# Kernel optimization log

Measured on AMD Instinct MI355X. Metric: run time of the kernel, lower is better.

## Reference

```python
import jax, jax.numpy as jnp
import numpy as np

ALPHA = 1.0
BETA = 1.0
NUM_BIAS_CLASSES = 2


def setup_inputs() -> dict:
    key = jax.random.key(0)
    k1, k2, k3, k4 = jax.random.split(key, 4)
    N, C, D = 4096, 10, 2048
    logits = jax.random.normal(k1, (N, C), dtype=jnp.float32)
    labels = jax.random.randint(k2, (N,), 0, C)
    biases = jax.random.randint(k3, (N,), 0, NUM_BIAS_CLASSES)
    feats = jax.random.normal(k4, (N, D), dtype=jnp.float32)
    return {"logits": logits, "labels": labels, "biases": biases, "feats": feats}


def reference(logits, labels, biases, feats):
    N = feats.shape[0]
    f32 = jnp.float32

    # ----- cross entropy (mean reduction, matches F.cross_entropy) -----
    logp = jax.nn.log_softmax(logits, axis=-1)
    label_loss = -jnp.mean(jnp.take_along_axis(logp, labels[:, None], axis=1))

    # ----- gram matrix: strict lower triangle of feats @ feats.T, clamped -----
    idx = jnp.arange(N)
    strict_lower = idx[:, None] > idx[None, :]            # [N, N] bool, i > j
    gram = jnp.matmul(feats, feats.T)                     # [N, N]
    gram = jnp.clip(jnp.where(strict_lower, gram, 0.0), -1.0, 1.0)

    # ----- R_ortho: per-bias-class |sum of gram over same-bias strict-lower pairs| -----
    # S_b = sum_{i>j, bias_i=bias_j=b} gram_ij = m_b^T gram m_b  (gram already strict lower)
    B = jax.nn.one_hot(biases, NUM_BIAS_CLASSES, dtype=f32)  # [N, NB]
    S = jnp.einsum('ib,ij,jb->b', B, gram, B)                # [NB]
    counts = jnp.sum(B, axis=0)                              # n_b per bias class
    M = counts * (counts - 1.0) * 0.5                        # strict-lower same-bias pairs
    M_tot_o = jnp.sum(M)
    # if M_b == 0 then S_b == 0, so summing all |S_b| matches the torch loop
    R_ortho = jnp.where(M_tot_o > 0, jnp.sum(jnp.abs(S)) / M_tot_o, 0.0)

    # ----- R_parallel: pairs i>j, same target, bias_i < bias_j (unique() is sorted,
    # so row-bias is the earlier-indexed class and col-bias the later one) -----
    same_target = labels[:, None] == labels[None, :]
    bias_lt = biases[:, None] < biases[None, :]
    pmask = (strict_lower & same_target & bias_lt).astype(f32)
    M_tot_p = jnp.sum(pmask)
    ploss = -0.5 * jnp.sum((1.0 + gram) * pmask)
    R_parallel = jnp.where(M_tot_p > 0, 1.0 + ploss / M_tot_p, 0.0)

    bias_loss = ALPHA * R_ortho + BETA * R_parallel
    return (label_loss, bias_loss)
```

## Files before the change

### kernel.cpp

```cpp
#include <hip/hip_runtime.h>
#include <hip/hip_bf16.h>

typedef short  bf16x8 __attribute__((ext_vector_type(8)));
typedef float  f32x4  __attribute__((ext_vector_type(4)));
typedef unsigned int uint2v __attribute__((ext_vector_type(2)));
typedef unsigned short ushort_t;

#define GLD_LDS16(gp, lp) __builtin_amdgcn_global_load_lds(                 \
    (const __attribute__((address_space(1))) void*)(gp),                    \
    (__attribute__((address_space(3))) void*)(lp), 16, 0, 0)

static __device__ inline short f2bf(float x) {
    unsigned u = __builtin_bit_cast(unsigned, x);
    u += 0x7fffu + ((u >> 16) & 1u);
    return (short)(u >> 16);
}

__global__ __launch_bounds__(256)
void convert_swz8_kernel(const float* __restrict__ in,
                         unsigned char* __restrict__ out,
                         int N, int D)
{
    int uid = blockIdx.x * blockDim.x + threadIdx.x;
    int nw  = D >> 3;
    if (uid >= N * nw) return;
    int row = uid / nw;
    int w   = uid - row * nw;
    int kt  = w >> 3;
    int p   = w & 7;
    int f   = p ^ (row & 7);
    int k   = kt * 64 + ((f >> 2) << 5) + ((f & 3) << 3);
    const float* s = in + (size_t)row * D + k;
    f32x4 a = *(const f32x4*)s;
    f32x4 b = *(const f32x4*)(s + 4);
    unsigned lo = __builtin_amdgcn_cvt_pk_fp8_f32(a[0], a[1], 0, 0);
    lo = __builtin_amdgcn_cvt_pk_fp8_f32(a[2], a[3], lo, 1);
    unsigned hi = __builtin_amdgcn_cvt_pk_fp8_f32(b[0], b[1], 0, 0);
    hi = __builtin_amdgcn_cvt_pk_fp8_f32(b[2], b[3], hi, 1);
    uint2v v = {lo, hi};
    *(uint2v*)(out + (size_t)uid * 8) = v;
}

__global__ __launch_bounds__(512, 1)
void gram_8phase8_kernel(const unsigned char* __restrict__ fb,
                         const int* __restrict__ labels,
                         const int* __restrict__ biases,
                         float* __restrict__ accbuf,
                         int N, int D)
{
    __shared__ unsigned char As[3][2][128][64];
    __shared__ unsigned char Bs[3][2][128][64];
    __shared__ int lab_r[256], bia_r[256], lab_c[256], bia_c[256];

    int nt = N >> 8;
    int b  = blockIdx.x;
    int nwg = gridDim.x;
    if ((nwg & 7) == 0) b = (b & 7) * (nwg >> 3) + (b >> 3);
    int r = b / nt, c = b % nt;
    int rowbase = r * 256, colbase = c * 256;

    int tid = threadIdx.x;
    if (tid < 256) {
        lab_r[tid] = labels[rowbase + tid];
        bia_r[tid] = biases[rowbase + tid];
    } else {
        int u = tid - 256;
        lab_c[u] = labels[colbase + u];
        bia_c[u] = biases[colbase + u];
    }

    int lane = tid & 63;
    int wid  = tid >> 6;
    int wr   = wid >> 2;
    int wc   = wid & 3;
    int lrow = lane & 15;
    int kgrp = lane >> 4;

    auto STAGE_A = [&](int slot, int h, int kt) {
        int row = tid >> 2;
        int blk = tid & 3;
        const unsigned char* g =
            fb + (size_t)(rowbase + h * 128 + row) * D + kt * 64 + blk * 16;
        GLD_LDS16(g, &As[slot][h][0][0] + tid * 16);
    };
    auto STAGE_B = [&](int slot, int h, int kt) {
        int row = tid >> 2;
        int blk = tid & 3;
        const unsigned char* g =
            fb + (size_t)(colbase + h * 128 + row) * D + kt * 64 + blk * 16;
        GLD_LDS16(g, &Bs[slot][h][0][0] + tid * 16);
    };

    f32x4 acc[8][4] = {};
    int nkt = D >> 6;

    STAGE_A(0, 0, 0); STAGE_A(0, 1, 0); STAGE_B(0, 0, 0); STAGE_B(0, 1, 0);
    STAGE_A(1, 0, 1); STAGE_A(1, 1, 1); STAGE_B(1, 0, 1); STAGE_B(1, 1, 1);
    asm volatile("s_waitcnt vmcnt(4)" ::: "memory");
    __builtin_amdgcn_s_barrier();

    int hb  = wc >> 1;
    int lcb = (wc & 1) * 64;

    int slot = 0, s2 = 2;
    for (int kt = 0; kt < nkt; ++kt) {
        int stg = (kt + 2 < nkt);
        unsigned long breg[4][2];

        #pragma unroll
        for (int q = 0; q < 4; ++q) {
            if (q == 0) {
                #pragma unroll
                for (int n = 0; n < 4; ++n)
                    #pragma unroll
                    for (int ks = 0; ks < 2; ++ks) {
                        int lc = lcb + n * 16 + lrow;
                        int u  = (ks * 4 + kgrp) ^ (lc & 7);
                        breg[n][ks] = *(const unsigned long*)(
                            &Bs[slot][hb][lc][0] + u * 8);
                    }
            }
            unsigned long areg[2][2];
            #pragma unroll
            for (int mm = 0; mm < 2; ++mm)
                #pragma unroll
                for (int ks = 0; ks < 2; ++ks) {
                    int lr = (q * 2 + mm) * 16 + lrow;
                    int u  = (ks * 4 + kgrp) ^ (lr & 7);
                    areg[mm][ks] = *(const unsigned long*)(
                        &As[slot][wr][lr][0] + u * 8);
                }
            if (stg) {
                if (q == 0)      STAGE_A(s2, 0, kt + 2);
                else if (q == 1) STAGE_A(s2, 1, kt + 2);
                else if (q == 2) STAGE_B(s2, 0, kt + 2);
                else             STAGE_B(s2, 1, kt + 2);
            }
            if (q == 3) {
                if (stg)
                    asm volatile("s_waitcnt vmcnt(4)" ::: "memory");
                else
                    asm volatile("s_waitcnt vmcnt(0)" ::: "memory");
            }
            __builtin_amdgcn_s_barrier();
            asm volatile("s_waitcnt lgkmcnt(0)" ::: "memory");
            __builtin_amdgcn_s_setprio(1);
            #pragma unroll
            for (int mm = 0; mm < 2; ++mm)
                #pragma unroll
                for (int n = 0; n < 4; ++n)
                    #pragma unroll
                    for (int ks = 0; ks < 2; ++ks)
                        acc[q * 2 + mm][n] =
                            __builtin_amdgcn_mfma_f32_16x16x32_fp8_fp8(
                                (long)areg[mm][ks], (long)breg[n][ks],
                                acc[q * 2 + mm][n], 0, 0, 0);
            __builtin_amdgcn_s_setprio(0);
            __builtin_amdgcn_s_barrier();
        }

        slot = (slot == 2) ? 0 : slot + 1;
        s2   = (s2   == 2) ? 0 : s2 + 1;
    }

    if (r < c) return;

    float s0 = 0.f, s1 = 0.f, ps = 0.f, pc = 0.f;
    #pragma unroll
    for (int m = 0; m < 8; ++m) {
        #pragma unroll
        for (int e = 0; e < 4; ++e) {
            int li = wr * 128 + m * 16 + kgrp * 4 + e;
            int gi = rowbase + li;
            int labi = lab_r[li];
            int bi   = bia_r[li];
            #pragma unroll
            for (int n = 0; n < 4; ++n) {
                int lj = wc * 64 + n * 16 + lrow;
                int gj = colbase + lj;
                if (gi > gj) {
                    float g = acc[m][n][e];
                    g = fminf(fmaxf(g, -1.f), 1.f);
                    int bj = bia_c[lj];
                    if (bi == bj) {
                        if (bi == 0) s0 += g; else s1 += g;
                    } else if (labi == lab_c[lj] && bi < bj) {
                        ps += 1.f + g;
                        pc += 1.f;
                    }
                }
            }
        }
    }
    #pragma unroll
    for (int off = 32; off > 0; off >>= 1) {
        s0 += __shfl_down(s0, off);
        s1 += __shfl_down(s1, off);
        ps += __shfl_down(ps, off);
        pc += __shfl_down(pc, off);
    }
    if (lane == 0) {
        atomicAdd(&accbuf[0], s0);
        atomicAdd(&accbuf[1], s1);
        atomicAdd(&accbuf[2], ps);
        atomicAdd(&accbuf[3], pc);
    }
}

__global__ __launch_bounds__(256, 2)
void gram_fused_kernel(const float* __restrict__ feats,
                       const int* __restrict__ labels,
                       const int* __restrict__ biases,
                       float* __restrict__ accbuf,
                       int N, int D)
{
    __shared__ ushort_t As[128 * 64];
    __shared__ ushort_t Bs[128 * 64];
    __shared__ int lab_r[128], bia_r[128], lab_c[128], bia_c[128];

    int t = blockIdx.x;
    int r = (int)((sqrtf(8.0f * (float)t + 1.0f) - 1.0f) * 0.5f);
    while ((r + 1) * (r + 2) / 2 <= t) ++r;
    while (r * (r + 1) / 2 > t) --r;
    int c = t - r * (r + 1) / 2;
    int rowbase = r * 128, colbase = c * 128;

    int tid = threadIdx.x;
    if (tid < 128) {
        lab_r[tid] = labels[rowbase + tid];
        bia_r[tid] = biases[rowbase + tid];
    } else {
        int u = tid - 128;
        lab_c[u] = labels[colbase + u];
        bia_c[u] = biases[colbase + u];
    }

    int lane = tid & 63;
    int wid  = tid >> 6;
    int wr   = wid >> 1;
    int wc   = wid & 1;
    int lrow = lane & 15;
    int kgrp = lane >> 4;

    f32x4 acc[4][4] = {};

    for (int k0 = 0; k0 < D; k0 += 64) {
        __syncthreads();
        #pragma unroll
        for (int it = 0; it < 4; ++it) {
            int wlin = tid + it * 256;
            int row  = wlin >> 3;
            int kc   = wlin & 7;
            const float* ga = feats + (size_t)(rowbase + row) * D + k0 + kc * 8;
            const float* gb = feats + (size_t)(colbase + row) * D + k0 + kc * 8;
            f32x4 a0 = *(const f32x4*)ga;
            f32x4 a1 = *(const f32x4*)(ga + 4);
            f32x4 b0 = *(const f32x4*)gb;
            f32x4 b1 = *(const f32x4*)(gb + 4);
            bf16x8 av, bv;
            #pragma unroll
            for (int e = 0; e < 4; ++e) {
                av[e]     = f2bf(a0[e]);
                av[e + 4] = f2bf(a1[e]);
                bv[e]     = f2bf(b0[e]);
                bv[e + 4] = f2bf(b1[e]);
            }
            int boff = row * 128 + ((kc * 16) ^ ((row & 7) << 4));
            *(bf16x8*)((char*)As + boff) = av;
            *(bf16x8*)((char*)Bs + boff) = bv;
        }
        __syncthreads();

        #pragma unroll
        for (int kk = 0; kk < 2; ++kk) {
            bf16x8 a[4], bb[4];
            #pragma unroll
            for (int m = 0; m < 4; ++m) {
                int rr = wr * 64 + m * 16 + lrow;
                int off = rr * 128 + ((kk * 64 + kgrp * 16) ^ ((rr & 7) << 4));
                a[m] = *(const bf16x8*)((const char*)As + off);
            }
            #pragma unroll
            for (int n = 0; n < 4; ++n) {
                int cc = wc * 64 + n * 16 + lrow;
                int off = cc * 128 + ((kk * 64 + kgrp * 16) ^ ((cc & 7) << 4));
                bb[n] = *(const bf16x8*)((const char*)Bs + off);
            }
            #pragma unroll
            for (int m = 0; m < 4; ++m)
                #pragma unroll
                for (int n = 0; n < 4; ++n)
                    acc[m][n] = __builtin_amdgcn_mfma_f32_16x16x32_bf16(
                        a[m], bb[n], acc[m][n], 0, 0, 0);
        }
    }

    float s0 = 0.f, s1 = 0.f, ps = 0.f, pc = 0.f;
    #pragma unroll
    for (int m = 0; m < 4; ++m) {
        #pragma unroll
        for (int e = 0; e < 4; ++e) {
            int li = wr * 64 + m * 16 + kgrp * 4 + e;
            int gi = rowbase + li;
            int labi = lab_r[li];
            int bi   = bia_r[li];
            #pragma unroll
            for (int n = 0; n < 4; ++n) {
                int lj = wc * 64 + n * 16 + lrow;
                int gj = colbase + lj;
                if (gi > gj) {
                    float g = acc[m][n][e];
                    g = fminf(fmaxf(g, -1.f), 1.f);
                    int bj = bia_c[lj];
                    if (bi == bj) {
                        if (bi == 0) s0 += g; else s1 += g;
                    } else if (labi == lab_c[lj] && bi < bj) {
                        ps += 1.f + g;
                        pc += 1.f;
                    }
                }
            }
        }
    }
    #pragma unroll
    for (int off = 32; off > 0; off >>= 1) {
        s0 += __shfl_down(s0, off);
        s1 += __shfl_down(s1, off);
        ps += __shfl_down(ps, off);
        pc += __shfl_down(pc, off);
    }
    if (lane == 0) {
        atomicAdd(&accbuf[0], s0);
        atomicAdd(&accbuf[1], s1);
        atomicAdd(&accbuf[2], ps);
        atomicAdd(&accbuf[3], pc);
    }
}

__global__ __launch_bounds__(256)
void ce_count_kernel(const float* __restrict__ logits,
                     const int* __restrict__ labels,
                     const int* __restrict__ biases,
                     float* __restrict__ accbuf,
                     int N, int C)
{
    int i = blockIdx.x * blockDim.x + threadIdx.x;
    float loss = 0.f, c0 = 0.f, c1 = 0.f;
    if (i < N) {
        const float* row = logits + (size_t)i * C;
        float mx = -INFINITY;
        for (int k = 0; k < C; ++k) mx = fmaxf(mx, row[k]);
        float s = 0.f;
        for (int k = 0; k < C; ++k) s += expf(row[k] - mx);
        loss = mx + logf(s) - row[labels[i]];
        if (biases[i] == 0) c0 = 1.f; else c1 = 1.f;
    }
    #pragma unroll
    for (int off = 32; off > 0; off >>= 1) {
        loss += __shfl_down(loss, off);
        c0   += __shfl_down(c0, off);
        c1   += __shfl_down(c1, off);
    }
    if ((threadIdx.x & 63) == 0) {
        atomicAdd(&accbuf[4], loss);
        atomicAdd(&accbuf[5], c0);
        atomicAdd(&accbuf[6], c1);
    }
}

__global__ void finalize_kernel(const float* __restrict__ accbuf,
                                float* __restrict__ out, int N)
{
    float S0 = accbuf[0], S1 = accbuf[1], ps = accbuf[2], pc = accbuf[3];
    float ce = accbuf[4], n0 = accbuf[5], n1 = accbuf[6];
    float Mo = 0.5f * (n0 * (n0 - 1.f) + n1 * (n1 - 1.f));
    float Ro = (Mo > 0.f) ? (fabsf(S0) + fabsf(S1)) / Mo : 0.f;
    float Rp = (pc > 0.f) ? 1.f + (-0.5f * ps) / pc : 0.f;
    out[0] = ce / (float)N;
    out[1] = Ro + Rp;
}

extern "C" void kernel_launch(void* const* d_in, const int* in_sizes, int n_in,
                              void* d_out, int out_size, void* d_ws, size_t ws_size,
                              hipStream_t stream)
{
    const float* logits = (const float*)d_in[0];
    const int*   labels = (const int*)d_in[1];
    const int*   biases = (const int*)d_in[2];
    const float* feats  = (const float*)d_in[3];

    int N = in_sizes[1];
    int C = in_sizes[0] / N;
    int D = in_sizes[3] / N;

    float* accbuf = (float*)d_ws;
    hipMemsetAsync(accbuf, 0, 8 * sizeof(float), stream);

    size_t need = 256 + (size_t)N * D;
    if (ws_size >= need && (N & 255) == 0 && (D & 127) == 0) {
        unsigned char* fb = (unsigned char*)d_ws + 256;
        int nu = N * (D >> 3);
        convert_swz8_kernel<<<(nu + 255) / 256, 256, 0, stream>>>(feats, fb,
                                                                  N, D);
        int nt = N >> 8;
        gram_8phase8_kernel<<<nt * nt, 512, 0, stream>>>(fb, labels, biases,
                                                         accbuf, N, D);
    } else {
        int nt = N / 128;
        int T  = nt * (nt + 1) / 2;
        gram_fused_kernel<<<T, 256, 0, stream>>>(feats, labels, biases, accbuf,
                                                 N, D);
    }
    ce_count_kernel<<<(N + 255) / 256, 256, 0, stream>>>(logits, labels, biases,
                                                         accbuf, N, C);
    finalize_kernel<<<1, 1, 0, stream>>>(accbuf, (float*)d_out, N);
}
```

Baseline: 142.6 us.

## Retile gram kernel to 256x128 blocks with 128-wide K steps

```diff
diff --git a/kernel.cpp b/kernel.cpp
--- a/kernel.cpp
+++ b/kernel.cpp
@@ -26,10 +26,10 @@
     if (uid >= N * nw) return;
     int row = uid / nw;
     int w   = uid - row * nw;
-    int kt  = w >> 3;
-    int p   = w & 7;
-    int f   = p ^ (row & 7);
-    int k   = kt * 64 + ((f >> 2) << 5) + ((f & 3) << 3);
+    int P   = w >> 4;
+    int p   = w & 15;
+    int f   = p ^ (row & 15);
+    int k   = P * 128 + ((f >> 2) << 5) + ((f & 3) << 3);
     const float* s = in + (size_t)row * D + k;
     f32x4 a = *(const f32x4*)s;
     f32x4 b = *(const f32x4*)(s + 4);
@@ -42,28 +42,28 @@
 }
 
 __global__ __launch_bounds__(512, 1)
-void gram_8phase8_kernel(const unsigned char* __restrict__ fb,
-                         const int* __restrict__ labels,
-                         const int* __restrict__ biases,
-                         float* __restrict__ accbuf,
-                         int N, int D)
-{
-    __shared__ unsigned char As[3][2][128][64];
-    __shared__ unsigned char Bs[3][2][128][64];
-    __shared__ int lab_r[256], bia_r[256], lab_c[256], bia_c[256];
-
-    int nt = N >> 8;
+void gram_p2_kernel(const unsigned char* __restrict__ fb,
+                    const int* __restrict__ labels,
+                    const int* __restrict__ biases,
+                    float* __restrict__ accbuf,
+                    int N, int D)
+{
+    __shared__ unsigned char As[3][256 * 128];
+    __shared__ unsigned char Bs[3][128 * 128];
+    __shared__ int lab_r[256], bia_r[256], lab_c[128], bia_c[128];
+
+    int nc = N >> 7;
     int b  = blockIdx.x;
     int nwg = gridDim.x;
     if ((nwg & 7) == 0) b = (b & 7) * (nwg >> 3) + (b >> 3);
-    int r = b / nt, c = b % nt;
-    int rowbase = r * 256, colbase = c * 256;
+    int r = b / nc, c = b % nc;
+    int rowbase = r * 256, colbase = c * 128;
 
     int tid = threadIdx.x;
     if (tid < 256) {
         lab_r[tid] = labels[rowbase + tid];
         bia_r[tid] = biases[rowbase + tid];
-    } else {
+    } else if (tid < 384) {
         int u = tid - 256;
         lab_c[u] = labels[colbase + u];
         bia_c[u] = biases[colbase + u];
@@ -71,106 +71,121 @@
 
     int lane = tid & 63;
     int wid  = tid >> 6;
-    int wr   = wid >> 2;
-    int wc   = wid & 3;
+    int wr   = wid >> 1;
+    int wc   = wid & 1;
     int lrow = lane & 15;
     int kgrp = lane >> 4;
 
-    auto STAGE_A = [&](int slot, int h, int kt) {
-        int row = tid >> 2;
-        int blk = tid & 3;
+    auto STAGE_A = [&](int slot, int kt, int i) {
+        int j   = i * 512 + tid;
+        int row = j >> 3;
+        int blk = j & 7;
         const unsigned char* g =
-            fb + (size_t)(rowbase + h * 128 + row) * D + kt * 64 + blk * 16;
-        GLD_LDS16(g, &As[slot][h][0][0] + tid * 16);
+            fb + (size_t)(rowbase + row) * D + kt * 128 + blk * 16;
+        GLD_LDS16(g, &As[slot][0] + j * 16);
     };
-    auto STAGE_B = [&](int slot, int h, int kt) {
-        int row = tid >> 2;
-        int blk = tid & 3;
+    auto STAGE_B = [&](int slot, int kt, int i) {
+        int j   = i * 512 + tid;
+        int row = j >> 3;
+        int blk = j & 7;
         const unsigned char* g =
-            fb + (size_t)(colbase + h * 128 + row) * D + kt * 64 + blk * 16;
-        GLD_LDS16(g, &Bs[slot][h][0][0] + tid * 16);
+            fb + (size_t)(colbase + row) * D + kt * 128 + blk * 16;
+        GLD_LDS16(g, &Bs[slot][0] + j * 16);
     };
 
-    f32x4 acc[8][4] = {};
-    int nkt = D >> 6;
-
-    STAGE_A(0, 0, 0); STAGE_A(0, 1, 0); STAGE_B(0, 0, 0); STAGE_B(0, 1, 0);
-    STAGE_A(1, 0, 1); STAGE_A(1, 1, 1); STAGE_B(1, 0, 1); STAGE_B(1, 1, 1);
-    asm volatile("s_waitcnt vmcnt(4)" ::: "memory");
+    f32x4 acc[4][4] = {};
+    int nkt = D >> 7;
+
+    STAGE_A(0, 0, 0); STAGE_A(0, 0, 1); STAGE_A(0, 0, 2); STAGE_A(0, 0, 3);
+    STAGE_B(0, 0, 0); STAGE_B(0, 0, 1);
+    STAGE_A(1, 1, 0); STAGE_A(1, 1, 1); STAGE_A(1, 1, 2); STAGE_A(1, 1, 3);
+    STAGE_B(1, 1, 0); STAGE_B(1, 1, 1);
+    asm volatile("s_waitcnt vmcnt(6)" ::: "memory");
     __builtin_amdgcn_s_barrier();
-
-    int hb  = wc >> 1;
-    int lcb = (wc & 1) * 64;
 
     int slot = 0, s2 = 2;
     for (int kt = 0; kt < nkt; ++kt) {
         int stg = (kt + 2 < nkt);
-        unsigned long breg[4][2];
-
-        #pragma unroll
-        for (int q = 0; q < 4; ++q) {
-            if (q == 0) {
+        unsigned long breg[4][4];
+        const unsigned char* Ab = &As[slot][0];
+        const unsigned char* Bb = &Bs[slot][0];
+
+        #pragma unroll
+        for (int n = 0; n < 4; ++n)
+            #pragma unroll
+            for (int ks = 0; ks < 4; ++ks) {
+                int lc = wc * 64 + n * 16 + lrow;
+                int u  = (ks * 4 + kgrp) ^ (lc & 15);
+                breg[n][ks] = *(const unsigned long*)(Bb + lc * 128 + u * 8);
+            }
+        unsigned long a0[2][4];
+        #pragma unroll
+        for (int mm = 0; mm < 2; ++mm)
+            #pragma unroll
+            for (int ks = 0; ks < 4; ++ks) {
+                int lr = wr * 64 + mm * 16 + lrow;
+                int u  = (ks * 4 + kgrp) ^ (lr & 15);
+                a0[mm][ks] = *(const unsigned long*)(Ab + lr * 128 + u * 8);
+            }
+        if (stg) { STAGE_A(s2, kt + 2, 0); STAGE_A(s2, kt + 2, 1);
+                   STAGE_A(s2, kt + 2, 2); }
+        __builtin_amdgcn_s_barrier();
+        asm volatile("s_waitcnt lgkmcnt(0)" ::: "memory");
+        __builtin_amdgcn_s_setprio(1);
+        #pragma unroll
+        for (int mm = 0; mm < 2; ++mm)
+            #pragma unroll
+            for (int n = 0; n < 4; ++n)
                 #pragma unroll
-                for (int n = 0; n < 4; ++n)
-                    #pragma unroll
-                    for (int ks = 0; ks < 2; ++ks) {
-                        int lc = lcb + n * 16 + lrow;
-                        int u  = (ks * 4 + kgrp) ^ (lc & 7);
-                        breg[n][ks] = *(const unsigned long*)(
-                            &Bs[slot][hb][lc][0] + u * 8);
-                    }
-            }
-            unsigned long areg[2][2];
-            #pragma unroll
-            for (int mm = 0; mm < 2; ++mm)
+                for (int ks = 0; ks < 4; ++ks)
+                    acc[mm][n] = __builtin_amdgcn_mfma_f32_16x16x32_fp8_fp8(
+                        (long)a0[mm][ks], (long)breg[n][ks], acc[mm][n],
+                        0, 0, 0);
+        __builtin_amdgcn_s_setprio(0);
+        __builtin_amdgcn_s_barrier();
+
+        unsigned long a1[2][4];
+        #pragma unroll
+        for (int mm = 0; mm < 2; ++mm)
+            #pragma unroll
+            for (int ks = 0; ks < 4; ++ks) {
+                int lr = wr * 64 + (2 + mm) * 16 + lrow;
+                int u  = (ks * 4 + kgrp) ^ (lr & 15);
+                a1[mm][ks] = *(const unsigned long*)(Ab + lr * 128 + u * 8);
+            }
+        if (stg) { STAGE_A(s2, kt + 2, 3); STAGE_B(s2, kt + 2, 0);
+                   STAGE_B(s2, kt + 2, 1); }
+        if (stg)
+            asm volatile("s_waitcnt vmcnt(6)" ::: "memory");
+        else
+            asm volatile("s_waitcnt vmcnt(0)" ::: "memory");
+        __builtin_amdgcn_s_barrier();
+        asm volatile("s_waitcnt lgkmcnt(0)" ::: "memory");
+        __builtin_amdgcn_s_setprio(1);
+        #pragma unroll
+        for (int mm = 0; mm < 2; ++mm)
+            #pragma unroll
+            for (int n = 0; n < 4; ++n)
                 #pragma unroll
-                for (int ks = 0; ks < 2; ++ks) {
-                    int lr = (q * 2 + mm) * 16 + lrow;
-                    int u  = (ks * 4 + kgrp) ^ (lr & 7);
-                    areg[mm][ks] = *(const unsigned long*)(
-                        &As[slot][wr][lr][0] + u * 8);
-                }
-            if (stg) {
-                if (q == 0)      STAGE_A(s2, 0, kt + 2);
-                else if (q == 1) STAGE_A(s2, 1, kt + 2);
-                else if (q == 2) STAGE_B(s2, 0, kt + 2);
-                else             STAGE_B(s2, 1, kt + 2);
-            }
-            if (q == 3) {
-                if (stg)
-                    asm volatile("s_waitcnt vmcnt(4)" ::: "memory");
-                else
-                    asm volatile("s_waitcnt vmcnt(0)" ::: "memory");
-            }
-            __builtin_amdgcn_s_barrier();
-            asm volatile("s_waitcnt lgkmcnt(0)" ::: "memory");
-            __builtin_amdgcn_s_setprio(1);
-            #pragma unroll
-            for (int mm = 0; mm < 2; ++mm)
-                #pragma unroll
-                for (int n = 0; n < 4; ++n)
-                    #pragma unroll
-                    for (int ks = 0; ks < 2; ++ks)
-                        acc[q * 2 + mm][n] =
-                            __builtin_amdgcn_mfma_f32_16x16x32_fp8_fp8(
-                                (long)areg[mm][ks], (long)breg[n][ks],
-                                acc[q * 2 + mm][n], 0, 0, 0);
-            __builtin_amdgcn_s_setprio(0);
-            __builtin_amdgcn_s_barrier();
-        }
+                for (int ks = 0; ks < 4; ++ks)
+                    acc[2 + mm][n] = __builtin_amdgcn_mfma_f32_16x16x32_fp8_fp8(
+                        (long)a1[mm][ks], (long)breg[n][ks], acc[2 + mm][n],
+                        0, 0, 0);
+        __builtin_amdgcn_s_setprio(0);
+        __builtin_amdgcn_s_barrier();
 
         slot = (slot == 2) ? 0 : slot + 1;
         s2   = (s2   == 2) ? 0 : s2 + 1;
     }
 
-    if (r < c) return;
+    if (rowbase + 255 <= colbase) return;
 
     float s0 = 0.f, s1 = 0.f, ps = 0.f, pc = 0.f;
     #pragma unroll
-    for (int m = 0; m < 8; ++m) {
+    for (int m = 0; m < 4; ++m) {
         #pragma unroll
         for (int e = 0; e < 4; ++e) {
-            int li = wr * 128 + m * 16 + kgrp * 4 + e;
+            int li = wr * 64 + m * 16 + kgrp * 4 + e;
             int gi = rowbase + li;
             int labi = lab_r[li];
             int bi   = bia_r[li];
@@ -402,9 +417,10 @@
         int nu = N * (D >> 3);
         convert_swz8_kernel<<<(nu + 255) / 256, 256, 0, stream>>>(feats, fb,
                                                                   N, D);
-        int nt = N >> 8;
-        gram_8phase8_kernel<<<nt * nt, 512, 0, stream>>>(fb, labels, biases,
-                                                         accbuf, N, D);
+        int nr = N >> 8;
+        int nc = N >> 7;
+        gram_p2_kernel<<<nr * nc, 512, 0, stream>>>(fb, labels, biases,
+                                                    accbuf, N, D);
     } else {
         int nt = N / 128;
         int T  = nt * (nt + 1) / 2;
```

Measured after the change: 178.9 us. 1.25x slower.

## Pair fp8 k-groups into 16-byte LDS reads and use a two-phase k-loop

Applied to the files above, without the earlier changes.

```diff
diff --git a/kernel.cpp b/kernel.cpp
--- a/kernel.cpp
+++ b/kernel.cpp
@@ -3,7 +3,8 @@
 
 typedef short  bf16x8 __attribute__((ext_vector_type(8)));
 typedef float  f32x4  __attribute__((ext_vector_type(4)));
-typedef unsigned int uint2v __attribute__((ext_vector_type(2)));
+typedef unsigned int uint4v __attribute__((ext_vector_type(4)));
+typedef unsigned long u64x2 __attribute__((ext_vector_type(2)));
 typedef unsigned short ushort_t;
 
 #define GLD_LDS16(gp, lp) __builtin_amdgcn_global_load_lds(                 \
@@ -17,36 +18,41 @@
 }
 
 __global__ __launch_bounds__(256)
-void convert_swz8_kernel(const float* __restrict__ in,
-                         unsigned char* __restrict__ out,
-                         int N, int D)
+void convert_pair8_kernel(const float* __restrict__ in,
+                          unsigned char* __restrict__ out,
+                          int N, int D)
 {
     int uid = blockIdx.x * blockDim.x + threadIdx.x;
-    int nw  = D >> 3;
+    int nw  = D >> 4;
     if (uid >= N * nw) return;
     int row = uid / nw;
     int w   = uid - row * nw;
-    int kt  = w >> 3;
-    int p   = w & 7;
-    int f   = p ^ (row & 7);
-    int k   = kt * 64 + ((f >> 2) << 5) + ((f & 3) << 3);
-    const float* s = in + (size_t)row * D + k;
-    f32x4 a = *(const f32x4*)s;
-    f32x4 b = *(const f32x4*)(s + 4);
-    unsigned lo = __builtin_amdgcn_cvt_pk_fp8_f32(a[0], a[1], 0, 0);
-    lo = __builtin_amdgcn_cvt_pk_fp8_f32(a[2], a[3], lo, 1);
-    unsigned hi = __builtin_amdgcn_cvt_pk_fp8_f32(b[0], b[1], 0, 0);
-    hi = __builtin_amdgcn_cvt_pk_fp8_f32(b[2], b[3], hi, 1);
-    uint2v v = {lo, hi};
-    *(uint2v*)(out + (size_t)uid * 8) = v;
+    int kt  = w >> 2;
+    int g   = w & 3;
+    int k0  = kt * 64 + g * 8;
+    const float* s = in + (size_t)row * D + k0;
+    f32x4 a0 = *(const f32x4*)s;
+    f32x4 a1 = *(const f32x4*)(s + 4);
+    f32x4 b0 = *(const f32x4*)(s + 32);
+    f32x4 b1 = *(const f32x4*)(s + 36);
+    unsigned w0 = __builtin_amdgcn_cvt_pk_fp8_f32(a0[0], a0[1], 0, 0);
+    w0 = __builtin_amdgcn_cvt_pk_fp8_f32(a0[2], a0[3], w0, 1);
+    unsigned w1 = __builtin_amdgcn_cvt_pk_fp8_f32(a1[0], a1[1], 0, 0);
+    w1 = __builtin_amdgcn_cvt_pk_fp8_f32(a1[2], a1[3], w1, 1);
+    unsigned w2 = __builtin_amdgcn_cvt_pk_fp8_f32(b0[0], b0[1], 0, 0);
+    w2 = __builtin_amdgcn_cvt_pk_fp8_f32(b0[2], b0[3], w2, 1);
+    unsigned w3 = __builtin_amdgcn_cvt_pk_fp8_f32(b1[0], b1[1], 0, 0);
+    w3 = __builtin_amdgcn_cvt_pk_fp8_f32(b1[2], b1[3], w3, 1);
+    uint4v v = {w0, w1, w2, w3};
+    *(uint4v*)(out + (size_t)uid * 16) = v;
 }
 
 __global__ __launch_bounds__(512, 1)
-void gram_8phase8_kernel(const unsigned char* __restrict__ fb,
-                         const int* __restrict__ labels,
-                         const int* __restrict__ biases,
-                         float* __restrict__ accbuf,
-                         int N, int D)
+void gram_p2k64_kernel(const unsigned char* __restrict__ fb,
+                       const int* __restrict__ labels,
+                       const int* __restrict__ biases,
+                       float* __restrict__ accbuf,
+                       int N, int D)
 {
     __shared__ unsigned char As[3][2][128][64];
     __shared__ unsigned char Bs[3][2][128][64];
@@ -105,59 +111,60 @@
     int slot = 0, s2 = 2;
     for (int kt = 0; kt < nkt; ++kt) {
         int stg = (kt + 2 < nkt);
-        unsigned long breg[4][2];
-
-        #pragma unroll
-        for (int q = 0; q < 4; ++q) {
-            if (q == 0) {
-                #pragma unroll
-                for (int n = 0; n < 4; ++n)
-                    #pragma unroll
-                    for (int ks = 0; ks < 2; ++ks) {
-                        int lc = lcb + n * 16 + lrow;
-                        int u  = (ks * 4 + kgrp) ^ (lc & 7);
-                        breg[n][ks] = *(const unsigned long*)(
-                            &Bs[slot][hb][lc][0] + u * 8);
-                    }
-            }
-            unsigned long areg[2][2];
-            #pragma unroll
-            for (int mm = 0; mm < 2; ++mm)
-                #pragma unroll
-                for (int ks = 0; ks < 2; ++ks) {
-                    int lr = (q * 2 + mm) * 16 + lrow;
-                    int u  = (ks * 4 + kgrp) ^ (lr & 7);
-                    areg[mm][ks] = *(const unsigned long*)(
-                        &As[slot][wr][lr][0] + u * 8);
-                }
-            if (stg) {
-                if (q == 0)      STAGE_A(s2, 0, kt + 2);
-                else if (q == 1) STAGE_A(s2, 1, kt + 2);
-                else if (q == 2) STAGE_B(s2, 0, kt + 2);
-                else             STAGE_B(s2, 1, kt + 2);
-            }
-            if (q == 3) {
-                if (stg)
-                    asm volatile("s_waitcnt vmcnt(4)" ::: "memory");
-                else
-                    asm volatile("s_waitcnt vmcnt(0)" ::: "memory");
-            }
-            __builtin_amdgcn_s_barrier();
-            asm volatile("s_waitcnt lgkmcnt(0)" ::: "memory");
-            __builtin_amdgcn_s_setprio(1);
-            #pragma unroll
-            for (int mm = 0; mm < 2; ++mm)
-                #pragma unroll
-                for (int n = 0; n < 4; ++n)
-                    #pragma unroll
-                    for (int ks = 0; ks < 2; ++ks)
-                        acc[q * 2 + mm][n] =
-                            __builtin_amdgcn_mfma_f32_16x16x32_fp8_fp8(
-                                (long)areg[mm][ks], (long)breg[n][ks],
-                                acc[q * 2 + mm][n], 0, 0, 0);
-            __builtin_amdgcn_s_setprio(0);
-            __builtin_amdgcn_s_barrier();
-        }
+        u64x2 breg[4];
+
+        #pragma unroll
+        for (int n = 0; n < 4; ++n) {
+            int lc = lcb + n * 16 + lrow;
+            breg[n] = *(const u64x2*)(&Bs[slot][hb][lc][0] + kgrp * 16);
+        }
+        u64x2 a0[4];
+        #pragma unroll
+        for (int mm = 0; mm < 4; ++mm) {
+            int lr = mm * 16 + lrow;
+            a0[mm] = *(const u64x2*)(&As[slot][wr][lr][0] + kgrp * 16);
+        }
+        if (stg) { STAGE_A(s2, 0, kt + 2); STAGE_A(s2, 1, kt + 2); }
+        __builtin_amdgcn_s_barrier();
+        asm volatile("s_waitcnt lgkmcnt(0)" ::: "memory");
+        __builtin_amdgcn_s_setprio(1);
+        #pragma unroll
+        for (int mm = 0; mm < 4; ++mm)
+            #pragma unroll
+            for (int n = 0; n < 4; ++n) {
+                acc[mm][n] = __builtin_amdgcn_mfma_f32_16x16x32_fp8_fp8(
+                    (long)a0[mm][0], (long)breg[n][0], acc[mm][n], 0, 0, 0);
+                acc[mm][n] = __builtin_amdgcn_mfma_f32_16x16x32_fp8_fp8(
+                    (long)a0[mm][1], (long)breg[n][1], acc[mm][n], 0, 0, 0);
+            }
+        __builtin_amdgcn_s_setprio(0);
+        __builtin_amdgcn_s_barrier();
+
+        u64x2 a1[4];
+        #pragma unroll
+        for (int mm = 0; mm < 4; ++mm) {
+            int lr = (4 + mm) * 16 + lrow;
+            a1[mm] = *(const u64x2*)(&As[slot][wr][lr][0] + kgrp * 16);
+        }
+        if (stg) { STAGE_B(s2, 0, kt + 2); STAGE_B(s2, 1, kt + 2); }
+        if (stg)
+            asm volatile("s_waitcnt vmcnt(4)" ::: "memory");
+        else
+            asm volatile("s_waitcnt vmcnt(0)" ::: "memory");
+        __builtin_amdgcn_s_barrier();
+        asm volatile("s_waitcnt lgkmcnt(0)" ::: "memory");
+        __builtin_amdgcn_s_setprio(1);
+        #pragma unroll
+        for (int mm = 0; mm < 4; ++mm)
+            #pragma unroll
+            for (int n = 0; n < 4; ++n) {
+                acc[4 + mm][n] = __builtin_amdgcn_mfma_f32_16x16x32_fp8_fp8(
+                    (long)a1[mm][0], (long)breg[n][0], acc[4 + mm][n], 0, 0, 0);
+                acc[4 + mm][n] = __builtin_amdgcn_mfma_f32_16x16x32_fp8_fp8(
+                    (long)a1[mm][1], (long)breg[n][1], acc[4 + mm][n], 0, 0, 0);
+            }
+        __builtin_amdgcn_s_setprio(0);
+        __builtin_amdgcn_s_barrier();
 
         slot = (slot == 2) ? 0 : slot + 1;
         s2   = (s2   == 2) ? 0 : s2 + 1;
@@ -397,14 +404,14 @@
     hipMemsetAsync(accbuf, 0, 8 * sizeof(float), stream);
 
     size_t need = 256 + (size_t)N * D;
-    if (ws_size >= need && (N & 255) == 0 && (D & 127) == 0) {
+    if (ws_size >= need && (N & 255) == 0 && (D & 63) == 0) {
         unsigned char* fb = (unsigned char*)d_ws + 256;
-        int nu = N * (D >> 3);
-        convert_swz8_kernel<<<(nu + 255) / 256, 256, 0, stream>>>(feats, fb,
-                                                                  N, D);
+        int nu = N * (D >> 4);
+        convert_pair8_kernel<<<(nu + 255) / 256, 256, 0, stream>>>(feats, fb,
+                                                                   N, D);
         int nt = N >> 8;
-        gram_8phase8_kernel<<<nt * nt, 512, 0, stream>>>(fb, labels, biases,
-                                                         accbuf, N, D);
+        gram_p2k64_kernel<<<nt * nt, 512, 0, stream>>>(fb, labels, biases,
+                                                       accbuf, N, D);
     } else {
         int nt = N / 128;
         int T  = nt * (nt + 1) / 2;
```

Result: faster. 137.1 us (-3.8%).
